# Performance work log

Hardware: AMD Instinct MI355X
Metric: run time of the kernel (lower is better)

Reference implementation:

```python
import jax, jax.numpy as jnp
import numpy as np

FEAT = 3136          # conved_channel//8 * pooled_size**2 = 512//8 * 7*7
HIDDEN = 64
NUM_CLASSES = 21
SELECTED_PROPOSAL = 128
LEAKY_SLOPE = 0.1


def leaky_relu(x, slope=LEAKY_SLOPE):
    return jnp.where(x >= 0, x, slope * x)


def setup_inputs() -> dict:
    key = jax.random.key(0)
    k_x, k_kc, k_w1, k_b1, k_w2, k_b2 = jax.random.split(key, 6)
    B, R = 64, 300
    x = jax.random.normal(k_x, (B, R, FEAT), dtype=jnp.float32)
    keep_count = jax.random.randint(k_kc, (B,), 0, R, dtype=jnp.int32)
    # nn.Linear default init: U(-1/sqrt(fan_in), 1/sqrt(fan_in))
    bnd1 = 1.0 / np.sqrt(FEAT)
    W1 = jax.random.uniform(k_w1, (FEAT, HIDDEN), jnp.float32, -bnd1, bnd1)
    b1 = jax.random.uniform(k_b1, (HIDDEN,), jnp.float32, -bnd1, bnd1)
    bnd2 = 1.0 / np.sqrt(HIDDEN)
    W2 = jax.random.uniform(k_w2, (HIDDEN, NUM_CLASSES), jnp.float32, -bnd2, bnd2)
    b2 = jax.random.uniform(k_b2, (NUM_CLASSES,), jnp.float32, -bnd2, bnd2)
    return {"x": x, "W1": W1, "b1": b1, "W2": W2, "b2": b2, "keep_count": keep_count}


def reference(x, W1, b1, W2, b2, keep_count):
    # x: [B, R, FEAT]; only the first SELECTED_PROPOSAL ROIs can be written.
    B = x.shape[0]
    S = SELECTED_PROPOSAL
    xs = x.reshape(B, x.shape[1], -1)[:, :S, :]                 # [B, S, F]
    h = leaky_relu(jnp.einsum('bsf,fh->bsh', xs, W1) + b1)      # [B, S, 64]
    # Dropout(0.25) is identity in eval mode.
    out = leaky_relu(jnp.einsum('bsh,hk->bsk', h, W2) + b2)     # [B, S, K]
    # rows j >= min(keep_count[idx], S) stay zero
    limit = jnp.minimum(keep_count, S)                          # [B]
    mask = jnp.arange(S)[None, :] < limit[:, None]              # [B, S]
    return jnp.where(mask[:, :, None], out, jnp.zeros((), out.dtype))
```

## Files before the change

kernel.cpp:

```cpp
#include <hip/hip_runtime.h>
#include <hip/hip_bf16.h>

static constexpr int FEAT_  = 3136;
static constexpr int KSTEPS = 98;
static constexpr int RSTR   = 300;
static constexpr int SROWS  = 128;
static constexpr int HID    = 64;
static constexpr int NCLS   = 21;

typedef __attribute__((ext_vector_type(8))) short bf16x8;
typedef __attribute__((ext_vector_type(4))) float f32x4;

__device__ bf16x8 g_w1p[KSTEPS * 4 * 64];

__device__ __forceinline__ short f2bf(float f) {
    union { float f; unsigned u; } v; v.f = f;
    unsigned r = v.u + 0x7fffu + ((v.u >> 16) & 1u);
    return (short)(r >> 16);
}

__global__ __launch_bounds__(256) void pack_w1(const float* __restrict__ W1) {
    int t = blockIdx.x * 256 + threadIdx.x;
    int lane = t & 63;
    int nt   = (t >> 6) & 3;
    int ks   = t >> 8;
    int col  = nt * 16 + (lane & 15);
    int k0   = ks * 32 + (lane >> 4) * 8;
    bf16x8 v;
    #pragma unroll
    for (int j = 0; j < 8; ++j) v[j] = f2bf(W1[(k0 + j) * HID + col]);
    g_w1p[t] = v;
}

__global__ __launch_bounds__(512) void fused_main(
    const float* __restrict__ x,  const float* __restrict__ b1,
    const float* __restrict__ W2, const float* __restrict__ b2,
    const int*  __restrict__ keep, float* __restrict__ out)
{
    const int tid  = threadIdx.x;
    const int lane = tid & 63;
    const int wv   = tid >> 6;
    const int row_base = blockIdx.x * 16;
    const int b      = row_base >> 7;
    const int s_base = row_base & 127;

    float* outp = out + row_base * NCLS;
    const int limit = min(keep[b], SROWS);

    if (s_base >= limit) {
        for (int i = tid; i < 16 * NCLS; i += 512) outp[i] = 0.f;
        return;
    }

    __shared__ float hp[8][16][HID + 1];
    __shared__ float hf[16][HID + 2];
    __shared__ float w2s[HID * NCLS];

    for (int i = tid; i < HID * NCLS; i += 512) w2s[i] = W2[i];

    const int ks0 = (wv * KSTEPS) >> 3;
    const int ks1 = ((wv + 1) * KSTEPS) >> 3;

    const int s_row = min(s_base + (lane & 15), limit - 1);
    const float* xp = x + (b * RSTR + s_row) * FEAT_ + ((lane >> 4) * 8);
    const bf16x8* wp = g_w1p + lane;

    f32x4 acc0 = {0.f,0.f,0.f,0.f}, acc1 = {0.f,0.f,0.f,0.f};
    f32x4 acc2 = {0.f,0.f,0.f,0.f}, acc3 = {0.f,0.f,0.f,0.f};

    #pragma unroll 2
    for (int ks = ks0; ks < ks1; ++ks) {
        float4 a0 = *(const float4*)(xp + ks * 32);
        float4 a1 = *(const float4*)(xp + ks * 32 + 4);
        bf16x8 bv0 = wp[(ks * 4 + 0) * 64];
        bf16x8 bv1 = wp[(ks * 4 + 1) * 64];
        bf16x8 bv2 = wp[(ks * 4 + 2) * 64];
        bf16x8 bv3 = wp[(ks * 4 + 3) * 64];
        bf16x8 af;
        af[0] = f2bf(a0.x); af[1] = f2bf(a0.y);
        af[2] = f2bf(a0.z); af[3] = f2bf(a0.w);
        af[4] = f2bf(a1.x); af[5] = f2bf(a1.y);
        af[6] = f2bf(a1.z); af[7] = f2bf(a1.w);
        acc0 = __builtin_amdgcn_mfma_f32_16x16x32_bf16(af, bv0, acc0, 0, 0, 0);
        acc1 = __builtin_amdgcn_mfma_f32_16x16x32_bf16(af, bv1, acc1, 0, 0, 0);
        acc2 = __builtin_amdgcn_mfma_f32_16x16x32_bf16(af, bv2, acc2, 0, 0, 0);
        acc3 = __builtin_amdgcn_mfma_f32_16x16x32_bf16(af, bv3, acc3, 0, 0, 0);
    }

    const int r0 = (lane >> 4) * 4;
    const int c0 = lane & 15;
    #pragma unroll
    for (int r = 0; r < 4; ++r) {
        hp[wv][r0 + r][c0     ] = acc0[r];
        hp[wv][r0 + r][c0 + 16] = acc1[r];
        hp[wv][r0 + r][c0 + 32] = acc2[r];
        hp[wv][r0 + r][c0 + 48] = acc3[r];
    }
    __syncthreads();

    for (int e = tid; e < 16 * HID; e += 512) {
        int row = e >> 6, col = e & 63;
        float v = b1[col];
        #pragma unroll
        for (int p = 0; p < 8; ++p) v += hp[p][row][col];
        hf[row][col] = (v >= 0.f) ? v : 0.1f * v;
    }
    __syncthreads();

    for (int idx = tid; idx < 16 * NCLS; idx += 512) {
        int r = idx / NCLS;
        int c = idx - r * NCLS;
        float a2 = b2[c];
        #pragma unroll 8
        for (int col = 0; col < HID; ++col)
            a2 += hf[r][col] * w2s[col * NCLS + c];
        a2 = (a2 >= 0.f) ? a2 : 0.1f * a2;
        outp[idx] = (s_base + r < limit) ? a2 : 0.f;
    }
}

extern "C" void kernel_launch(void* const* d_in, const int* in_sizes, int n_in,
                              void* d_out, int out_size, void* d_ws, size_t ws_size,
                              hipStream_t stream) {
    const float* x    = (const float*)d_in[0];
    const float* W1   = (const float*)d_in[1];
    const float* b1   = (const float*)d_in[2];
    const float* W2   = (const float*)d_in[3];
    const float* b2   = (const float*)d_in[4];
    const int*   keep = (const int*)d_in[5];
    float* out = (float*)d_out;

    hipLaunchKernelGGL(pack_w1,    dim3(KSTEPS), dim3(256), 0, stream, W1);
    hipLaunchKernelGGL(fused_main, dim3((64 * SROWS) / 16), dim3(512), 0, stream,
                       x, b1, W2, b2, keep, out);
}
```

Measured before the change: 31.84 us.

## Process 32 rows per block to reuse W1 fragments across two MFMA tiles

Each block now covers 32 proposal rows instead of 16. Every wave issues two 16-row MFMA tiles per k-step that share the same loaded W1 fragments, which halves W1 traffic per row. The K ordering inside each 32-wide step is permuted to two float4 chunks spaced 16 apart, and pack_w1 is changed to match. The grid is halved to 256 blocks, which lowers parallelism and coarsens the early-exit granularity for masked rows.

```diff
diff --git a/kernel.cpp b/kernel.cpp
--- a/kernel.cpp
+++ b/kernel.cpp
@@ -7,6 +7,7 @@
 static constexpr int SROWS  = 128;
 static constexpr int HID    = 64;
 static constexpr int NCLS   = 21;
+static constexpr int BM     = 32;
 
 typedef __attribute__((ext_vector_type(8))) short bf16x8;
 typedef __attribute__((ext_vector_type(4))) float f32x4;
@@ -25,10 +26,13 @@
     int nt   = (t >> 6) & 3;
     int ks   = t >> 8;
     int col  = nt * 16 + (lane & 15);
-    int k0   = ks * 32 + (lane >> 4) * 8;
+    int g    = lane >> 4;
+    int k0   = ks * 32 + g * 4;
     bf16x8 v;
     #pragma unroll
-    for (int j = 0; j < 8; ++j) v[j] = f2bf(W1[(k0 + j) * HID + col]);
+    for (int j = 0; j < 4; ++j) v[j]     = f2bf(W1[(k0 + j) * HID + col]);
+    #pragma unroll
+    for (int j = 0; j < 4; ++j) v[4 + j] = f2bf(W1[(k0 + 16 + j) * HID + col]);
     g_w1p[t] = v;
 }
 
@@ -40,7 +44,7 @@
     const int tid  = threadIdx.x;
     const int lane = tid & 63;
     const int wv   = tid >> 6;
-    const int row_base = blockIdx.x * 16;
+    const int row_base = blockIdx.x * BM;
     const int b      = row_base >> 7;
     const int s_base = row_base & 127;
 
@@ -48,12 +52,12 @@
     const int limit = min(keep[b], SROWS);
 
     if (s_base >= limit) {
-        for (int i = tid; i < 16 * NCLS; i += 512) outp[i] = 0.f;
+        for (int i = tid; i < BM * NCLS; i += 512) outp[i] = 0.f;
         return;
     }
 
-    __shared__ float hp[8][16][HID + 1];
-    __shared__ float hf[16][HID + 2];
+    __shared__ float hp[8][BM][HID + 1];
+    __shared__ float hf[BM][HID + 2];
     __shared__ float w2s[HID * NCLS];
 
     for (int i = tid; i < HID * NCLS; i += 512) w2s[i] = W2[i];
@@ -61,44 +65,57 @@
     const int ks0 = (wv * KSTEPS) >> 3;
     const int ks1 = ((wv + 1) * KSTEPS) >> 3;
 
-    const int s_row = min(s_base + (lane & 15), limit - 1);
-    const float* xp = x + (b * RSTR + s_row) * FEAT_ + ((lane >> 4) * 8);
+    const int g = lane >> 4;
+    const int r = lane & 15;
+    const int row0 = min(s_base + r,      limit - 1);
+    const int row1 = min(s_base + 16 + r, limit - 1);
+    const float* xp0 = x + (b * RSTR + row0) * FEAT_ + g * 4;
+    const float* xp1 = x + (b * RSTR + row1) * FEAT_ + g * 4;
     const bf16x8* wp = g_w1p + lane;
 
-    f32x4 acc0 = {0.f,0.f,0.f,0.f}, acc1 = {0.f,0.f,0.f,0.f};
-    f32x4 acc2 = {0.f,0.f,0.f,0.f}, acc3 = {0.f,0.f,0.f,0.f};
+    f32x4 a00 = {0,0,0,0}, a01 = {0,0,0,0}, a02 = {0,0,0,0}, a03 = {0,0,0,0};
+    f32x4 a10 = {0,0,0,0}, a11 = {0,0,0,0}, a12 = {0,0,0,0}, a13 = {0,0,0,0};
 
     #pragma unroll 2
     for (int ks = ks0; ks < ks1; ++ks) {
-        float4 a0 = *(const float4*)(xp + ks * 32);
-        float4 a1 = *(const float4*)(xp + ks * 32 + 4);
+        float4 p0a = *(const float4*)(xp0 + ks * 32);
+        float4 p0b = *(const float4*)(xp0 + ks * 32 + 16);
+        float4 p1a = *(const float4*)(xp1 + ks * 32);
+        float4 p1b = *(const float4*)(xp1 + ks * 32 + 16);
         bf16x8 bv0 = wp[(ks * 4 + 0) * 64];
         bf16x8 bv1 = wp[(ks * 4 + 1) * 64];
         bf16x8 bv2 = wp[(ks * 4 + 2) * 64];
         bf16x8 bv3 = wp[(ks * 4 + 3) * 64];
-        bf16x8 af;
-        af[0] = f2bf(a0.x); af[1] = f2bf(a0.y);
-        af[2] = f2bf(a0.z); af[3] = f2bf(a0.w);
-        af[4] = f2bf(a1.x); af[5] = f2bf(a1.y);
-        af[6] = f2bf(a1.z); af[7] = f2bf(a1.w);
-        acc0 = __builtin_amdgcn_mfma_f32_16x16x32_bf16(af, bv0, acc0, 0, 0, 0);
-        acc1 = __builtin_amdgcn_mfma_f32_16x16x32_bf16(af, bv1, acc1, 0, 0, 0);
-        acc2 = __builtin_amdgcn_mfma_f32_16x16x32_bf16(af, bv2, acc2, 0, 0, 0);
-        acc3 = __builtin_amdgcn_mfma_f32_16x16x32_bf16(af, bv3, acc3, 0, 0, 0);
+        bf16x8 af0, af1;
+        af0[0]=f2bf(p0a.x); af0[1]=f2bf(p0a.y); af0[2]=f2bf(p0a.z); af0[3]=f2bf(p0a.w);
+        af0[4]=f2bf(p0b.x); af0[5]=f2bf(p0b.y); af0[6]=f2bf(p0b.z); af0[7]=f2bf(p0b.w);
+        af1[0]=f2bf(p1a.x); af1[1]=f2bf(p1a.y); af1[2]=f2bf(p1a.z); af1[3]=f2bf(p1a.w);
+        af1[4]=f2bf(p1b.x); af1[5]=f2bf(p1b.y); af1[6]=f2bf(p1b.z); af1[7]=f2bf(p1b.w);
+        a00 = __builtin_amdgcn_mfma_f32_16x16x32_bf16(af0, bv0, a00, 0, 0, 0);
+        a01 = __builtin_amdgcn_mfma_f32_16x16x32_bf16(af0, bv1, a01, 0, 0, 0);
+        a02 = __builtin_amdgcn_mfma_f32_16x16x32_bf16(af0, bv2, a02, 0, 0, 0);
+        a03 = __builtin_amdgcn_mfma_f32_16x16x32_bf16(af0, bv3, a03, 0, 0, 0);
+        a10 = __builtin_amdgcn_mfma_f32_16x16x32_bf16(af1, bv0, a10, 0, 0, 0);
+        a11 = __builtin_amdgcn_mfma_f32_16x16x32_bf16(af1, bv1, a11, 0, 0, 0);
+        a12 = __builtin_amdgcn_mfma_f32_16x16x32_bf16(af1, bv2, a12, 0, 0, 0);
+        a13 = __builtin_amdgcn_mfma_f32_16x16x32_bf16(af1, bv3, a13, 0, 0, 0);
     }
 
-    const int r0 = (lane >> 4) * 4;
-    const int c0 = lane & 15;
     #pragma unroll
-    for (int r = 0; r < 4; ++r) {
-        hp[wv][r0 + r][c0     ] = acc0[r];
-        hp[wv][r0 + r][c0 + 16] = acc1[r];
-        hp[wv][r0 + r][c0 + 32] = acc2[r];
-        hp[wv][r0 + r][c0 + 48] = acc3[r];
+    for (int rr = 0; rr < 4; ++rr) {
+        const int mr0 = g * 4 + rr, mr1 = 16 + g * 4 + rr;
+        hp[wv][mr0][r     ] = a00[rr];
+        hp[wv][mr0][r + 16] = a01[rr];
+        hp[wv][mr0][r + 32] = a02[rr];
+        hp[wv][mr0][r + 48] = a03[rr];
+        hp[wv][mr1][r     ] = a10[rr];
+        hp[wv][mr1][r + 16] = a11[rr];
+        hp[wv][mr1][r + 32] = a12[rr];
+        hp[wv][mr1][r + 48] = a13[rr];
     }
     __syncthreads();
 
-    for (int e = tid; e < 16 * HID; e += 512) {
+    for (int e = tid; e < BM * HID; e += 512) {
         int row = e >> 6, col = e & 63;
         float v = b1[col];
         #pragma unroll
@@ -107,15 +124,15 @@
     }
     __syncthreads();
 
-    for (int idx = tid; idx < 16 * NCLS; idx += 512) {
-        int r = idx / NCLS;
-        int c = idx - r * NCLS;
+    for (int idx = tid; idx < BM * NCLS; idx += 512) {
+        int rI = idx / NCLS;
+        int c  = idx - rI * NCLS;
         float a2 = b2[c];
         #pragma unroll 8
         for (int col = 0; col < HID; ++col)
-            a2 += hf[r][col] * w2s[col * NCLS + c];
+            a2 += hf[rI][col] * w2s[col * NCLS + c];
         a2 = (a2 >= 0.f) ? a2 : 0.1f * a2;
-        outp[idx] = (s_base + r < limit) ? a2 : 0.f;
+        outp[idx] = (s_base + rI < limit) ? a2 : 0.f;
     }
 }
 
@@ -131,6 +148,6 @@
     float* out = (float*)d_out;
 
     hipLaunchKernelGGL(pack_w1,    dim3(KSTEPS), dim3(256), 0, stream, W1);
-    hipLaunchKernelGGL(fused_main, dim3((64 * SROWS) / 16), dim3(512), 0, stream,
+    hipLaunchKernelGGL(fused_main, dim3((64 * SROWS) / BM), dim3(512), 0, stream,
                        x, b1, W2, b2, keep, out);
 }
```

New measurement: 29.03 us. 8.8% less time.
